# Kernel tuning notes

Measured on AMD Instinct MI355X. Metric: run time of the kernel, lower is better.

Reference implementation:

```python
import jax, jax.numpy as jnp
import numpy as np

D = 768
H = 8
DH = D // H
EPS = 1e-5

def _layer_norm(x, g, b):
    mu = jnp.mean(x, axis=-1, keepdims=True)
    var = jnp.mean(jnp.square(x - mu), axis=-1, keepdims=True)
    return (x - mu) * jax.lax.rsqrt(var + EPS) * g + b

def _mha_seq1(xq, xkv, w_in, b_in, w_out, b_out):
    # torch MultiheadAttention with seq_len=1 on both query and key/value.
    # xq, xkv: [B, D]; w_in: [3D, D]; w_out: [D, D]
    B = xq.shape[0]
    q = xq @ w_in[:D].T + b_in[:D]
    k = xkv @ w_in[D:2 * D].T + b_in[D:2 * D]
    v = xkv @ w_in[2 * D:].T + b_in[2 * D:]
    q = q.reshape(B, H, DH)
    k = k.reshape(B, H, DH)
    v = v.reshape(B, H, DH)
    s = jnp.sum(q * k, axis=-1, keepdims=True) / jnp.sqrt(jnp.float32(DH))  # [B,H,1]
    a = jax.nn.softmax(s[..., None], axis=-1)[..., 0]  # softmax over single key -> ones
    out = (a * v).reshape(B, D)
    return out @ w_out.T + b_out

def setup_inputs() -> dict:
    key = jax.random.key(0)
    ks = jax.random.split(key, 16)
    B = 8192
    s = 0.02
    inp = {
        "query_feat": jax.random.normal(ks[0], (B, D), jnp.float32),
        "ref_feat": jax.random.normal(ks[1], (B, D), jnp.float32),
        # self-attention MHA
        "sa_w_in": jax.random.normal(ks[2], (3 * D, D), jnp.float32) * s,
        "sa_b_in": jnp.zeros((3 * D,), jnp.float32),
        "sa_w_out": jax.random.normal(ks[3], (D, D), jnp.float32) * s,
        "sa_b_out": jnp.zeros((D,), jnp.float32),
        "ln1_g": jnp.ones((D,), jnp.float32),
        "ln1_b": jnp.zeros((D,), jnp.float32),
        # cross-attention MHA
        "ca_w_in": jax.random.normal(ks[4], (3 * D, D), jnp.float32) * s,
        "ca_b_in": jnp.zeros((3 * D,), jnp.float32),
        "ca_w_out": jax.random.normal(ks[5], (D, D), jnp.float32) * s,
        "ca_b_out": jnp.zeros((D,), jnp.float32),
        "ln2_g": jnp.ones((D,), jnp.float32),
        "ln2_b": jnp.zeros((D,), jnp.float32),
        # MLP
        "mlp_w1": jax.random.normal(ks[6], (D, D), jnp.float32) * s,
        "mlp_b1": jnp.zeros((D,), jnp.float32),
        "mlp_w2": jax.random.normal(ks[7], (512, D), jnp.float32) * s,
        "mlp_b2": jnp.zeros((512,), jnp.float32),
    }
    return inp

def reference(query_feat, ref_feat, sa_w_in, sa_b_in, sa_w_out, sa_b_out,
              ln1_g, ln1_b, ca_w_in, ca_b_in, ca_w_out, ca_b_out,
              ln2_g, ln2_b, mlp_w1, mlp_b1, mlp_w2, mlp_b2):
    # self-attention block (seq_len = 1)
    q = _mha_seq1(query_feat, query_feat, sa_w_in, sa_b_in, sa_w_out, sa_b_out)
    q = _layer_norm(query_feat + q, ln1_g, ln1_b)
    # cross-attention block
    x = _mha_seq1(q, ref_feat, ca_w_in, ca_b_in, ca_w_out, ca_b_out)
    x = _layer_norm(q + x, ln2_g, ln2_b)
    # relu -> dropout(eval: identity) -> mean over seq dim of size 1 (identity)
    x = jax.nn.relu(x)
    # MLP: Linear(768,768) -> ReLU -> Linear(768,512) -> ReLU
    x = jax.nn.relu(x @ mlp_w1.T + mlp_b1)
    x = jax.nn.relu(x @ mlp_w2.T + mlp_b2)
    return x
```

## Files before the change

kernel.cpp:

```cpp
#include <hip/hip_runtime.h>
#include <stdint.h>

typedef unsigned short u16;
typedef __bf16 bf16x8 __attribute__((ext_vector_type(8)));
typedef float f32x4 __attribute__((ext_vector_type(4)));

#define DD 768
#define LN_EPS 1e-5f

__device__ __forceinline__ u16 f2bf(float f) {
  union { float f; unsigned u; } x; x.f = f;
  unsigned r = x.u + 0x7fffu + ((x.u >> 16) & 1u);
  return (u16)(r >> 16);
}
__device__ __forceinline__ float bf2f(u16 h) {
  union { unsigned u; float f; } x; x.u = ((unsigned)h) << 16; return x.f;
}

__device__ __forceinline__ void async16(void* ldsp, const void* g) {
  __builtin_amdgcn_global_load_lds(
      (const __attribute__((address_space(1))) void*)g,
      (__attribute__((address_space(3))) void*)ldsp,
      16, 0, 0);
}

template<int MODE, int NF>
__device__ __forceinline__ void gemm_body(
    const u16* __restrict__ A, const u16* __restrict__ W,
    const float* __restrict__ bias, const u16* __restrict__ Rbf,
    void* __restrict__ Out, int M, int N, int K)
{
  const int BN = NF * 32;
  const int STRIDE = 16384 + BN * 128;
  __shared__ char lds[2 * (16384 + NF * 32 * 128)];
  const int tid  = threadIdx.x;
  const int lane = tid & 63;
  const int wid  = tid >> 6;
  const int wm = wid >> 1, wn = wid & 1;
  const int row0 = blockIdx.x * 128;
  const int col0 = blockIdx.y * BN;
  const int l15 = lane & 15;
  const int l4  = lane >> 4;

  f32x4 acc[4][NF];
  const f32x4 zero4 = {0.f, 0.f, 0.f, 0.f};
#pragma unroll
  for (int m = 0; m < 4; ++m)
#pragma unroll
    for (int n = 0; n < NF; ++n) acc[m][n] = zero4;

  int aoff[2][4], boff[2][NF];
#pragma unroll
  for (int ks = 0; ks < 2; ++ks) {
#pragma unroll
    for (int m = 0; m < 4; ++m) {
      int ra = wm * 64 + m * 16 + l15;
      aoff[ks][m] = ra * 128 + (((ks * 4 + l4) ^ (ra & 7)) * 16);
    }
#pragma unroll
    for (int n = 0; n < NF; ++n) {
      int rb = wn * (NF * 16) + n * 16 + l15;
      boff[ks][n] = 16384 + rb * 128 + (((ks * 4 + l4) ^ (rb & 7)) * 16);
    }
  }

  const int NC = NF > 4 ? NF : 4;
  int rr[NC], cbp[NC];
#pragma unroll
  for (int c = 0; c < NC; ++c) {
    rr[c]  = c * 32 + (tid >> 3);
    cbp[c] = ((tid & 7) ^ (rr[c] & 7)) * 8;
  }
  const size_t abase = (size_t)row0 * K;
  const size_t wbase = (size_t)col0 * K;

  auto STAGE = [&](int buf, int kt) {
    char* bA = lds + buf * STRIDE + wid * 1024;
    char* bB = lds + buf * STRIDE + 16384 + wid * 1024;
#pragma unroll
    for (int c = 0; c < 4; ++c)
      async16(bA + c * 4096, A + abase + (size_t)rr[c] * K + kt + cbp[c]);
#pragma unroll
    for (int c = 0; c < NF; ++c)
      async16(bB + c * 4096, W + wbase + (size_t)rr[c] * K + kt + cbp[c]);
  };
  auto COMPUTE = [&](int buf) {
    const char* base = lds + buf * STRIDE;
#pragma unroll
    for (int ks = 0; ks < 2; ++ks) {
      bf16x8 af[4], bfr[NF];
#pragma unroll
      for (int m = 0; m < 4; ++m)  af[m]  = *(const bf16x8*)(base + aoff[ks][m]);
#pragma unroll
      for (int n = 0; n < NF; ++n) bfr[n] = *(const bf16x8*)(base + boff[ks][n]);
      __builtin_amdgcn_s_setprio(1);
#pragma unroll
      for (int m = 0; m < 4; ++m)
#pragma unroll
        for (int n = 0; n < NF; ++n)
          acc[m][n] = __builtin_amdgcn_mfma_f32_16x16x32_bf16(
              af[m], bfr[n], acc[m][n], 0, 0, 0);
      __builtin_amdgcn_s_setprio(0);
    }
  };

  STAGE(0, 0);
  __syncthreads();
  int cur = 0;
  for (int kt = 64; kt < K; kt += 64) {
    STAGE(cur ^ 1, kt);
    COMPUTE(cur);
    __syncthreads();
    cur ^= 1;
  }
  COMPUTE(cur);

  float bcol[NF];
#pragma unroll
  for (int n = 0; n < NF; ++n)
    bcol[n] = (MODE == 0) ? 0.f : bias[col0 + wn * (NF * 16) + n * 16 + l15];

#pragma unroll
  for (int m = 0; m < 4; ++m) {
    int r0 = row0 + wm * 64 + m * 16 + l4 * 4;
#pragma unroll
    for (int n = 0; n < NF; ++n) {
      int c = col0 + wn * (NF * 16) + n * 16 + l15;
#pragma unroll
      for (int j = 0; j < 4; ++j) {
        size_t idx = (size_t)(r0 + j) * N + c;
        float v = acc[m][n][j];
        if (MODE == 0) {
          ((u16*)Out)[idx] = f2bf(v);
        } else if (MODE == 1) {
          v += bcol[n];
          if (Rbf) v += bf2f(Rbf[idx]);
          ((u16*)Out)[idx] = f2bf(v);
        } else if (MODE == 2) {
          ((u16*)Out)[idx] = f2bf(fmaxf(v + bcol[n], 0.f));
        } else {
          ((float*)Out)[idx] = fmaxf(v + bcol[n], 0.f);
        }
      }
    }
  }
}

__global__ __launch_bounds__(256) void k_gemm_fuse(
    const u16* WoSa, const u16* WvTSa, u16* WsaF,
    const u16* WoCa, const u16* WvTCa, u16* WcaF)
{
  int z = blockIdx.z;
  gemm_body<0, 4>(z ? WoCa : WoSa, z ? WvTCa : WvTSa, nullptr, nullptr,
                  z ? WcaF : WsaF, DD, DD, DD);
}

__global__ __launch_bounds__(256) void k_gemm_att(
    const u16* qfb, const u16* rfb, const u16* WsaF, const u16* WcaF,
    const float* bsa, const float* bca,
    u16* t1, u16* ca, int M)
{
  int z = blockIdx.z;
  gemm_body<1, 3>(z ? rfb : qfb, z ? WcaF : WsaF, z ? bca : bsa,
                  z ? (const u16*)nullptr : qfb,
                  z ? (void*)ca : (void*)t1, M, DD, DD);
}

__global__ __launch_bounds__(256) void k_mlp1(
    const u16* xb, const u16* W1, const float* b1, u16* hb, int M)
{ gemm_body<2, 3>(xb, W1, b1, nullptr, hb, M, DD, DD); }

__global__ __launch_bounds__(256) void k_mlp2(
    const u16* hb, const u16* W2, const float* b2, float* out, int M)
{ gemm_body<3, 2>(hb, W2, b2, nullptr, out, M, 512, DD); }

__global__ __launch_bounds__(256) void k_prep(
    const float* sa_w_v, u16* WvTSaB, const float* ca_w_v, u16* WvTCaB,
    const float* WoSa, const float* bvSa, const float* boSa, float* bsaF,
    const float* WoCa, const float* bvCa, const float* boCa, float* bcaF,
    const float* s0, u16* d0, int n0, const float* s1, u16* d1, int n1,
    const float* s2, u16* d2, int n2, const float* s3, u16* d3, int n3,
    const float* s4, u16* d4, int n4, const float* s5, u16* d5, int n5)
{
  __shared__ float t[32][33];
  const int b = blockIdx.x;
  const int tid = threadIdx.x;

  if (b < 1152) {
    int z = b / 576, r = b % 576;
    const float* src = z ? ca_w_v : sa_w_v;
    u16* dst = z ? WvTCaB : WvTSaB;
    int by = (r / 24) * 32, bx = (r % 24) * 32;
    int x = tid & 31, y4 = tid >> 5;
#pragma unroll
    for (int i = 0; i < 32; i += 8)
      t[y4 + i][x] = src[(size_t)(by + y4 + i) * DD + bx + x];
    __syncthreads();
#pragma unroll
    for (int i = 0; i < 32; i += 8)
      dst[(size_t)(bx + y4 + i) * DD + by + x] = f2bf(t[x][y4 + i]);
    return;
  }
  if (b < 1536) {
    int bb = b - 1152;
    const float *Wo, *bv, *bo; float* out;
    if (bb < 192) { Wo = WoSa; bv = bvSa; bo = boSa; out = bsaF; }
    else          { Wo = WoCa; bv = bvCa; bo = boCa; out = bcaF; bb -= 192; }
    int lane = tid & 63;
    int n = bb * 4 + (tid >> 6);
    float s = 0.f;
    for (int k = lane; k < DD; k += 64) s += Wo[(size_t)n * DD + k] * bv[k];
#pragma unroll
    for (int o = 32; o > 0; o >>= 1) s += __shfl_down(s, o, 64);
    if (lane == 0) out[n] = s + bo[n];
    return;
  }
  int total = n0 + n1 + n2 + n3 + n4 + n5;
  int nblk = gridDim.x - 1536;
  for (int i = (b - 1536) * 256 + tid; i < total; i += nblk * 256) {
    int j = i; const float* s; u16* d;
    if (j < n0) { s = s0; d = d0; }
    else { j -= n0;
      if (j < n1) { s = s1; d = d1; }
      else { j -= n1;
        if (j < n2) { s = s2; d = d2; }
        else { j -= n2;
          if (j < n3) { s = s3; d = d3; }
          else { j -= n3;
            if (j < n4) { s = s4; d = d4; }
            else { j -= n4; s = s5; d = d5; }
          }
        }
      }
    }
    float4 v = ((const float4*)s)[j];
    ushort4 o;
    o.x = f2bf(v.x); o.y = f2bf(v.y); o.z = f2bf(v.z); o.w = f2bf(v.w);
    ((ushort4*)d)[j] = o;
  }
}

__global__ __launch_bounds__(256) void k_ln(
    const u16* __restrict__ t1, const u16* __restrict__ caB,
    const float* __restrict__ g1, const float* __restrict__ b1,
    const float* __restrict__ g2, const float* __restrict__ b2,
    u16* __restrict__ xout, int M)
{
  int row = blockIdx.x * 4 + (threadIdx.x >> 6);
  int lane = threadIdx.x & 63;
  const ushort4* p1 = (const ushort4*)(t1 + (size_t)row * DD);
  const ushort4* pc = (const ushort4*)(caB + (size_t)row * DD);
  const float4* pg1 = (const float4*)g1; const float4* pb1 = (const float4*)b1;
  const float4* pg2 = (const float4*)g2; const float4* pb2 = (const float4*)b2;

  float v[12];
  float s = 0.f, s2 = 0.f;
#pragma unroll
  for (int i = 0; i < 3; ++i) {
    ushort4 q = p1[lane + 64 * i];
    float a0 = bf2f(q.x), a1 = bf2f(q.y), a2 = bf2f(q.z), a3 = bf2f(q.w);
    v[i*4+0] = a0; v[i*4+1] = a1; v[i*4+2] = a2; v[i*4+3] = a3;
    s  += a0 + a1 + a2 + a3;
    s2 += a0*a0 + a1*a1 + a2*a2 + a3*a3;
  }
#pragma unroll
  for (int o = 32; o > 0; o >>= 1) { s += __shfl_xor(s, o, 64); s2 += __shfl_xor(s2, o, 64); }
  float mu = s * (1.f / DD);
  float rs = rsqrtf(s2 * (1.f / DD) - mu * mu + LN_EPS);

  float y[12];
  s = 0.f; s2 = 0.f;
#pragma unroll
  for (int i = 0; i < 3; ++i) {
    float4 gg = pg1[lane + 64 * i]; float4 bb = pb1[lane + 64 * i];
    ushort4 cc = pc[lane + 64 * i];
    float y0 = (v[i*4+0] - mu) * rs * gg.x + bb.x + bf2f(cc.x);
    float y1 = (v[i*4+1] - mu) * rs * gg.y + bb.y + bf2f(cc.y);
    float y2 = (v[i*4+2] - mu) * rs * gg.z + bb.z + bf2f(cc.z);
    float y3 = (v[i*4+3] - mu) * rs * gg.w + bb.w + bf2f(cc.w);
    y[i*4+0] = y0; y[i*4+1] = y1; y[i*4+2] = y2; y[i*4+3] = y3;
    s  += y0 + y1 + y2 + y3;
    s2 += y0*y0 + y1*y1 + y2*y2 + y3*y3;
  }
#pragma unroll
  for (int o = 32; o > 0; o >>= 1) { s += __shfl_xor(s, o, 64); s2 += __shfl_xor(s2, o, 64); }
  float mu2 = s * (1.f / DD);
  float rs2 = rsqrtf(s2 * (1.f / DD) - mu2 * mu2 + LN_EPS);

  ushort4* po = (ushort4*)(xout + (size_t)row * DD);
#pragma unroll
  for (int i = 0; i < 3; ++i) {
    float4 gg = pg2[lane + 64 * i]; float4 bb = pb2[lane + 64 * i];
    ushort4 o;
    o.x = f2bf(fmaxf((y[i*4+0] - mu2) * rs2 * gg.x + bb.x, 0.f));
    o.y = f2bf(fmaxf((y[i*4+1] - mu2) * rs2 * gg.y + bb.y, 0.f));
    o.z = f2bf(fmaxf((y[i*4+2] - mu2) * rs2 * gg.z + bb.z, 0.f));
    o.w = f2bf(fmaxf((y[i*4+3] - mu2) * rs2 * gg.w + bb.w, 0.f));
    po[lane + 64 * i] = o;
  }
}

extern "C" void kernel_launch(void* const* d_in, const int* in_sizes, int n_in,
                              void* d_out, int out_size, void* d_ws, size_t ws_size,
                              hipStream_t stream) {
  const float* query    = (const float*)d_in[0];
  const float* ref      = (const float*)d_in[1];
  const float* sa_w_in  = (const float*)d_in[2];
  const float* sa_b_in  = (const float*)d_in[3];
  const float* sa_w_out = (const float*)d_in[4];
  const float* sa_b_out = (const float*)d_in[5];
  const float* ln1_g    = (const float*)d_in[6];
  const float* ln1_b    = (const float*)d_in[7];
  const float* ca_w_in  = (const float*)d_in[8];
  const float* ca_b_in  = (const float*)d_in[9];
  const float* ca_w_out = (const float*)d_in[10];
  const float* ca_b_out = (const float*)d_in[11];
  const float* ln2_g    = (const float*)d_in[12];
  const float* ln2_b    = (const float*)d_in[13];
  const float* w1       = (const float*)d_in[14];
  const float* b1       = (const float*)d_in[15];
  const float* w2       = (const float*)d_in[16];
  const float* b2       = (const float*)d_in[17];
  const int M = in_sizes[0] / DD;

  char* p = (char*)d_ws;
  u16* qf_bf = (u16*)p; p += (size_t)M * DD * 2;
  u16* rf_bf = (u16*)p; p += (size_t)M * DD * 2;
  u16* t1    = (u16*)p; p += (size_t)M * DD * 2;
  u16* ca    = (u16*)p; p += (size_t)M * DD * 2;
  u16* WoSaB  = (u16*)p; p += DD * DD * 2;
  u16* WoCaB  = (u16*)p; p += DD * DD * 2;
  u16* WvTSaB = (u16*)p; p += DD * DD * 2;
  u16* WvTCaB = (u16*)p; p += DD * DD * 2;
  u16* W1b    = (u16*)p; p += DD * DD * 2;
  u16* W2b    = (u16*)p; p += 512 * DD * 2;
  u16* WsaF   = (u16*)p; p += DD * DD * 2;
  u16* WcaF   = (u16*)p; p += DD * DD * 2;
  float* bsaF = (float*)p; p += DD * 4;
  float* bcaF = (float*)p; p += DD * 4;

  const int nf  = M * DD / 4;
  const int nw  = DD * DD / 4;
  const int nw2 = 512 * DD / 4;

  k_prep<<<dim3(1536 + 1536), 256, 0, stream>>>(
      sa_w_in + 2 * DD * DD, WvTSaB, ca_w_in + 2 * DD * DD, WvTCaB,
      sa_w_out, sa_b_in + 2 * DD, sa_b_out, bsaF,
      ca_w_out, ca_b_in + 2 * DD, ca_b_out, bcaF,
      query, qf_bf, nf, ref, rf_bf, nf,
      sa_w_out, WoSaB, nw, ca_w_out, WoCaB, nw,
      w1, W1b, nw, w2, W2b, nw2);

  k_gemm_fuse<<<dim3(6, 6, 2), 256, 0, stream>>>(
      WoSaB, WvTSaB, WsaF, WoCaB, WvTCaB, WcaF);

  k_gemm_att<<<dim3(M / 128, 8, 2), 256, 0, stream>>>(
      qf_bf, rf_bf, WsaF, WcaF, bsaF, bcaF, t1, ca, M);

  k_ln<<<dim3(M / 4), 256, 0, stream>>>(
      t1, ca, ln1_g, ln1_b, ln2_g, ln2_b, rf_bf, M);

  k_mlp1<<<dim3(M / 128, 8), 256, 0, stream>>>(rf_bf, W1b, b1, qf_bf, M);

  k_mlp2<<<dim3(M / 128, 8), 256, 0, stream>>>(qf_bf, W2b, b2, (float*)d_out, M);
}
```

Before: 96.52 us.

## Add triple-buffered GEMM pipeline with single barrier for attention and MLP2

Adds a gemm_pipe3 variant that keeps three LDS stages in flight, using explicit vmcnt waits and one barrier per K-step instead of double buffering with two syncs. The attention GEMM and MLP2 switch to it, and the attention GEMM also narrows its N tile from 96 to 64 columns with a 12-wide grid. The aim is to hide global-to-LDS latency and raise block count. The cost is more LDS per block, which can lower occupancy, and the hand-written waitcnt values depend on exactly how many loads each stage issues.

Result: slower. 100.0 us (+3.6%).

```diff
diff --git a/kernel.cpp b/kernel.cpp
--- a/kernel.cpp
+++ b/kernel.cpp
@@ -24,15 +24,16 @@
       16, 0, 0);
 }
 
+
 template<int MODE, int NF>
-__device__ __forceinline__ void gemm_body(
+__device__ __forceinline__ void gemm_pipe3(
     const u16* __restrict__ A, const u16* __restrict__ W,
     const float* __restrict__ bias, const u16* __restrict__ Rbf,
     void* __restrict__ Out, int M, int N, int K)
 {
   const int BN = NF * 32;
   const int STRIDE = 16384 + BN * 128;
-  __shared__ char lds[2 * (16384 + NF * 32 * 128)];
+  __shared__ char lds[3 * (16384 + NF * 32 * 128)];
   const int tid  = threadIdx.x;
   const int lane = tid & 63;
   const int wid  = tid >> 6;
@@ -41,6 +42,7 @@
   const int col0 = blockIdx.y * BN;
   const int l15 = lane & 15;
   const int l4  = lane >> 4;
+  const int NT = K / 64;
 
   f32x4 acc[4][NF];
   const f32x4 zero4 = {0.f, 0.f, 0.f, 0.f};
@@ -105,15 +107,23 @@
   };
 
   STAGE(0, 0);
-  __syncthreads();
-  int cur = 0;
-  for (int kt = 64; kt < K; kt += 64) {
-    STAGE(cur ^ 1, kt);
+  STAGE(1, 64);
+  int cur = 0, nxt = 2;
+#pragma unroll 1
+  for (int t = 0; t < NT; ++t) {
+    if (t < NT - 1) {
+      asm volatile("s_waitcnt vmcnt(6)" ::: "memory");
+    } else {
+      asm volatile("s_waitcnt vmcnt(0)" ::: "memory");
+    }
+    __builtin_amdgcn_s_barrier();
+    if (t + 2 < NT) {
+      STAGE(nxt, (t + 2) * 64);
+      nxt = (nxt == 2) ? 0 : nxt + 1;
+    }
     COMPUTE(cur);
-    __syncthreads();
-    cur ^= 1;
-  }
-  COMPUTE(cur);
+    cur = (cur == 2) ? 0 : cur + 1;
+  }
 
   float bcol[NF];
 #pragma unroll
@@ -146,6 +156,128 @@
   }
 }
 
+template<int MODE, int NF>
+__device__ __forceinline__ void gemm_body(
+    const u16* __restrict__ A, const u16* __restrict__ W,
+    const float* __restrict__ bias, const u16* __restrict__ Rbf,
+    void* __restrict__ Out, int M, int N, int K)
+{
+  const int BN = NF * 32;
+  const int STRIDE = 16384 + BN * 128;
+  __shared__ char lds[2 * (16384 + NF * 32 * 128)];
+  const int tid  = threadIdx.x;
+  const int lane = tid & 63;
+  const int wid  = tid >> 6;
+  const int wm = wid >> 1, wn = wid & 1;
+  const int row0 = blockIdx.x * 128;
+  const int col0 = blockIdx.y * BN;
+  const int l15 = lane & 15;
+  const int l4  = lane >> 4;
+
+  f32x4 acc[4][NF];
+  const f32x4 zero4 = {0.f, 0.f, 0.f, 0.f};
+#pragma unroll
+  for (int m = 0; m < 4; ++m)
+#pragma unroll
+    for (int n = 0; n < NF; ++n) acc[m][n] = zero4;
+
+  int aoff[2][4], boff[2][NF];
+#pragma unroll
+  for (int ks = 0; ks < 2; ++ks) {
+#pragma unroll
+    for (int m = 0; m < 4; ++m) {
+      int ra = wm * 64 + m * 16 + l15;
+      aoff[ks][m] = ra * 128 + (((ks * 4 + l4) ^ (ra & 7)) * 16);
+    }
+#pragma unroll
+    for (int n = 0; n < NF; ++n) {
+      int rb = wn * (NF * 16) + n * 16 + l15;
+      boff[ks][n] = 16384 + rb * 128 + (((ks * 4 + l4) ^ (rb & 7)) * 16);
+    }
+  }
+
+  const int NC = NF > 4 ? NF : 4;
+  int rr[NC], cbp[NC];
+#pragma unroll
+  for (int c = 0; c < NC; ++c) {
+    rr[c]  = c * 32 + (tid >> 3);
+    cbp[c] = ((tid & 7) ^ (rr[c] & 7)) * 8;
+  }
+  const size_t abase = (size_t)row0 * K;
+  const size_t wbase = (size_t)col0 * K;
+
+  auto STAGE = [&](int buf, int kt) {
+    char* bA = lds + buf * STRIDE + wid * 1024;
+    char* bB = lds + buf * STRIDE + 16384 + wid * 1024;
+#pragma unroll
+    for (int c = 0; c < 4; ++c)
+      async16(bA + c * 4096, A + abase + (size_t)rr[c] * K + kt + cbp[c]);
+#pragma unroll
+    for (int c = 0; c < NF; ++c)
+      async16(bB + c * 4096, W + wbase + (size_t)rr[c] * K + kt + cbp[c]);
+  };
+  auto COMPUTE = [&](int buf) {
+    const char* base = lds + buf * STRIDE;
+#pragma unroll
+    for (int ks = 0; ks < 2; ++ks) {
+      bf16x8 af[4], bfr[NF];
+#pragma unroll
+      for (int m = 0; m < 4; ++m)  af[m]  = *(const bf16x8*)(base + aoff[ks][m]);
+#pragma unroll
+      for (int n = 0; n < NF; ++n) bfr[n] = *(const bf16x8*)(base + boff[ks][n]);
+      __builtin_amdgcn_s_setprio(1);
+#pragma unroll
+      for (int m = 0; m < 4; ++m)
+#pragma unroll
+        for (int n = 0; n < NF; ++n)
+          acc[m][n] = __builtin_amdgcn_mfma_f32_16x16x32_bf16(
+              af[m], bfr[n], acc[m][n], 0, 0, 0);
+      __builtin_amdgcn_s_setprio(0);
+    }
+  };
+
+  STAGE(0, 0);
+  __syncthreads();
+  int cur = 0;
+  for (int kt = 64; kt < K; kt += 64) {
+    STAGE(cur ^ 1, kt);
+    COMPUTE(cur);
+    __syncthreads();
+    cur ^= 1;
+  }
+  COMPUTE(cur);
+
+  float bcol[NF];
+#pragma unroll
+  for (int n = 0; n < NF; ++n)
+    bcol[n] = (MODE == 0) ? 0.f : bias[col0 + wn * (NF * 16) + n * 16 + l15];
+
+#pragma unroll
+  for (int m = 0; m < 4; ++m) {
+    int r0 = row0 + wm * 64 + m * 16 + l4 * 4;
+#pragma unroll
+    for (int n = 0; n < NF; ++n) {
+      int c = col0 + wn * (NF * 16) + n * 16 + l15;
+#pragma unroll
+      for (int j = 0; j < 4; ++j) {
+        size_t idx = (size_t)(r0 + j) * N + c;
+        float v = acc[m][n][j];
+        if (MODE == 0) {
+          ((u16*)Out)[idx] = f2bf(v);
+        } else if (MODE == 1) {
+          v += bcol[n];
+          if (Rbf) v += bf2f(Rbf[idx]);
+          ((u16*)Out)[idx] = f2bf(v);
+        } else if (MODE == 2) {
+          ((u16*)Out)[idx] = f2bf(fmaxf(v + bcol[n], 0.f));
+        } else {
+          ((float*)Out)[idx] = fmaxf(v + bcol[n], 0.f);
+        }
+      }
+    }
+  }
+}
+
 __global__ __launch_bounds__(256) void k_gemm_fuse(
     const u16* WoSa, const u16* WvTSa, u16* WsaF,
     const u16* WoCa, const u16* WvTCa, u16* WcaF)
@@ -161,9 +293,9 @@
     u16* t1, u16* ca, int M)
 {
   int z = blockIdx.z;
-  gemm_body<1, 3>(z ? rfb : qfb, z ? WcaF : WsaF, z ? bca : bsa,
-                  z ? (const u16*)nullptr : qfb,
-                  z ? (void*)ca : (void*)t1, M, DD, DD);
+  gemm_pipe3<1, 2>(z ? rfb : qfb, z ? WcaF : WsaF, z ? bca : bsa,
+                   z ? (const u16*)nullptr : qfb,
+                   z ? (void*)ca : (void*)t1, M, DD, DD);
 }
 
 __global__ __launch_bounds__(256) void k_mlp1(
@@ -172,7 +304,7 @@
 
 __global__ __launch_bounds__(256) void k_mlp2(
     const u16* hb, const u16* W2, const float* b2, float* out, int M)
-{ gemm_body<3, 2>(hb, W2, b2, nullptr, out, M, 512, DD); }
+{ gemm_pipe3<3, 2>(hb, W2, b2, nullptr, out, M, 512, DD); }
 
 __global__ __launch_bounds__(256) void k_prep(
     const float* sa_w_v, u16* WvTSaB, const float* ca_w_v, u16* WvTCaB,
@@ -354,7 +486,7 @@
   k_gemm_fuse<<<dim3(6, 6, 2), 256, 0, stream>>>(
       WoSaB, WvTSaB, WsaF, WoCaB, WvTCaB, WcaF);
 
-  k_gemm_att<<<dim3(M / 128, 8, 2), 256, 0, stream>>>(
+  k_gemm_att<<<dim3(M / 128, 12, 2), 256, 0, stream>>>(
       qf_bf, rf_bf, WsaF, WcaF, bsaF, bcaF, t1, ca, M);
 
   k_ln<<<dim3(M / 4), 256, 0, stream>>>(
```
